# Kernel optimization log

Measured on AMD Instinct MI355X. Metric: run time of the kernel, lower is better.

The kernel has to match this reference:

```python
import jax, jax.numpy as jnp
import numpy as np


def _compute_wavelet(scaling_rec):
    # g_k = h_{M-k-1}, with sign flip on odd indices (note: torch code flips
    # first, then negates odd indices of the flipped filter).
    g = jnp.flip(scaling_rec, axis=-1)
    signs = jnp.where(jnp.arange(g.shape[-1]) % 2 == 1, -1.0, 1.0).astype(g.dtype)
    return g * signs


def _convolve(x, filt):
    # Circular convolution via rFFT, matching torch.fft.rfft/irfft semantics.
    n = x.shape[-1]
    ra = jnp.fft.rfft(x)
    rb = jnp.fft.rfft(filt, n=n)
    return jnp.fft.irfft(ra * rb, n=n).astype(x.dtype)


def setup_inputs() -> dict:
    key = jax.random.key(0)
    k1, k2, k3 = jax.random.split(key, 3)
    inp = jax.random.normal(k1, (4096, 8192), dtype=jnp.float32)
    scaling = jax.random.normal(k2, (8,), dtype=jnp.float32)
    scaling_rec = jax.random.normal(k3, (8,), dtype=jnp.float32)
    return {"input": inp, "scaling": scaling, "scaling_rec": scaling_rec}


def reference(input, scaling, scaling_rec):
    wavelet = _compute_wavelet(scaling_rec)
    even = input[:, ::2]   # (n, m/2)
    odd = input[:, 1::2]   # (n, m/2)
    odd_updated = odd - _convolve(even, wavelet)
    even_updated = even - _convolve(odd, scaling)
    return (even_updated, odd_updated)
```

## Files before the change

kernel.cpp:

```cpp
#include <hip/hip_runtime.h>


#define COLS       8192
#define HALF       4096
#define F4_PER_ROW 2048
#define NTHREADS   256

__global__ __launch_bounds__(NTHREADS) void fwd_dwt_kernel(
    const float* __restrict__ input,
    const float* __restrict__ scaling,
    const float* __restrict__ scaling_rec,
    float* __restrict__ out,
    int rows)
{
    const int t   = blockIdx.x * NTHREADS + threadIdx.x;
    const int row = t >> 11;
    const int f   = t & (F4_PER_ROW - 1);

    const float4* in4 = (const float4*)(input + (size_t)row * COLS);

    float w[8], sc[8];
#pragma unroll
    for (int j = 0; j < 8; ++j) {
        w[j]  = scaling_rec[7 - j] * ((j & 1) ? -1.0f : 1.0f);
        sc[j] = scaling[j];
    }

    const float4 v  = in4[f];
    const float4 h1 = in4[(f - 1) & (F4_PER_ROW - 1)];
    const float4 h2 = in4[(f - 2) & (F4_PER_ROW - 1)];
    const float4 h3 = in4[(f - 3) & (F4_PER_ROW - 1)];
    const float4 h4 = in4[(f - 4) & (F4_PER_ROW - 1)];

    float pe[9], po[9];
    pe[0] = h4.z; po[0] = h4.w;
    pe[1] = h3.x; po[1] = h3.y;  pe[2] = h3.z; po[2] = h3.w;
    pe[3] = h2.x; po[3] = h2.y;  pe[4] = h2.z; po[4] = h2.w;
    pe[5] = h1.x; po[5] = h1.y;  pe[6] = h1.z; po[6] = h1.w;
    pe[7] = v.x;  po[7] = v.y;   pe[8] = v.z;  po[8] = v.w;

    float eo0 = pe[7], oo0 = po[7], eo1 = pe[8], oo1 = po[8];
#pragma unroll
    for (int j = 0; j < 8; ++j) {
        eo0 -= po[7 - j] * sc[j];
        oo0 -= pe[7 - j] * w[j];
        eo1 -= po[8 - j] * sc[j];
        oo1 -= pe[8 - j] * w[j];
    }

    float* oe = out + (size_t)row * HALF + 2 * f;
    float* od = out + (size_t)rows * HALF + (size_t)row * HALF + 2 * f;
    ((float2*)oe)[0] = make_float2(eo0, eo1);
    ((float2*)od)[0] = make_float2(oo0, oo1);
}

extern "C" void kernel_launch(void* const* d_in, const int* in_sizes, int n_in,
                              void* d_out, int out_size, void* d_ws, size_t ws_size,
                              hipStream_t stream) {
    const float* input       = (const float*)d_in[0];
    const float* scaling     = (const float*)d_in[1];
    const float* scaling_rec = (const float*)d_in[2];
    float*       out         = (float*)d_out;

    const int rows    = in_sizes[0] / COLS;
    const int threads = rows * F4_PER_ROW;
    fwd_dwt_kernel<<<threads / NTHREADS, NTHREADS, 0, stream>>>(
        input, scaling, scaling_rec, out, rows);
}
```

Before: 228.7 us.

## Process multiple rows per thread with double-buffered register prefetch

Each thread now handles 16 rows strided by rows/16 instead of one. The next row's five float4 loads are issued before computing the current one, giving a software-pipelined double buffer in registers. The goal is to cut grid size, amortise filter-coefficient loads and index math, and keep more memory requests in flight per thread. In exchange the grid is 16x smaller, which lowers wave-level parallelism and raises register use. The code assumes rows is divisible by 16.

```diff
diff --git a/kernel.cpp b/kernel.cpp
--- a/kernel.cpp
+++ b/kernel.cpp
@@ -5,6 +5,7 @@
 #define HALF       4096
 #define F4_PER_ROW 2048
 #define NTHREADS   256
+#define ITERS      16
 
 __global__ __launch_bounds__(NTHREADS) void fwd_dwt_kernel(
     const float* __restrict__ input,
@@ -13,11 +14,15 @@
     float* __restrict__ out,
     int rows)
 {
-    const int t   = blockIdx.x * NTHREADS + threadIdx.x;
-    const int row = t >> 11;
-    const int f   = t & (F4_PER_ROW - 1);
+    const int g       = blockIdx.x * NTHREADS + threadIdx.x;
+    const int f       = g & (F4_PER_ROW - 1);
+    const int rowbase = g >> 11;
+    const int rs      = rows / ITERS;
 
-    const float4* in4 = (const float4*)(input + (size_t)row * COLS);
+    const int m1 = (f - 1) & (F4_PER_ROW - 1);
+    const int m2 = (f - 2) & (F4_PER_ROW - 1);
+    const int m3 = (f - 3) & (F4_PER_ROW - 1);
+    const int m4 = (f - 4) & (F4_PER_ROW - 1);
 
     float w[8], sc[8];
 #pragma unroll
@@ -26,32 +31,62 @@
         sc[j] = scaling[j];
     }
 
-    const float4 v  = in4[f];
-    const float4 h1 = in4[(f - 1) & (F4_PER_ROW - 1)];
-    const float4 h2 = in4[(f - 2) & (F4_PER_ROW - 1)];
-    const float4 h3 = in4[(f - 3) & (F4_PER_ROW - 1)];
-    const float4 h4 = in4[(f - 4) & (F4_PER_ROW - 1)];
+    struct W5 { float4 v, h1, h2, h3, h4; };
 
-    float pe[9], po[9];
-    pe[0] = h4.z; po[0] = h4.w;
-    pe[1] = h3.x; po[1] = h3.y;  pe[2] = h3.z; po[2] = h3.w;
-    pe[3] = h2.x; po[3] = h2.y;  pe[4] = h2.z; po[4] = h2.w;
-    pe[5] = h1.x; po[5] = h1.y;  pe[6] = h1.z; po[6] = h1.w;
-    pe[7] = v.x;  po[7] = v.y;   pe[8] = v.z;  po[8] = v.w;
+    auto LOAD = [&](const float4* base) {
+        W5 r;
+        r.v  = base[f];
+        r.h1 = base[m1];
+        r.h2 = base[m2];
+        r.h3 = base[m3];
+        r.h4 = base[m4];
+        return r;
+    };
 
-    float eo0 = pe[7], oo0 = po[7], eo1 = pe[8], oo1 = po[8];
+    auto CRUNCH = [&](const W5& x, float* poe, float* pod) {
+        float pe[9], po[9];
+        pe[0] = x.h4.z; po[0] = x.h4.w;
+        pe[1] = x.h3.x; po[1] = x.h3.y;  pe[2] = x.h3.z; po[2] = x.h3.w;
+        pe[3] = x.h2.x; po[3] = x.h2.y;  pe[4] = x.h2.z; po[4] = x.h2.w;
+        pe[5] = x.h1.x; po[5] = x.h1.y;  pe[6] = x.h1.z; po[6] = x.h1.w;
+        pe[7] = x.v.x;  po[7] = x.v.y;   pe[8] = x.v.z;  po[8] = x.v.w;
+
+        float eo0 = pe[7], oo0 = po[7], eo1 = pe[8], oo1 = po[8];
 #pragma unroll
-    for (int j = 0; j < 8; ++j) {
-        eo0 -= po[7 - j] * sc[j];
-        oo0 -= pe[7 - j] * w[j];
-        eo1 -= po[8 - j] * sc[j];
-        oo1 -= pe[8 - j] * w[j];
+        for (int j = 0; j < 8; ++j) {
+            eo0 -= po[7 - j] * sc[j];
+            oo0 -= pe[7 - j] * w[j];
+            eo1 -= po[8 - j] * sc[j];
+            oo1 -= pe[8 - j] * w[j];
+        }
+        ((float2*)poe)[0] = make_float2(eo0, eo1);
+        ((float2*)pod)[0] = make_float2(oo0, oo1);
+    };
+
+    const size_t in_step  = (size_t)rs * F4_PER_ROW;
+    const size_t out_step = (size_t)rs * HALF;
+
+    const float4* ip = (const float4*)input + (size_t)rowbase * F4_PER_ROW;
+    float* pe = out + (size_t)rowbase * HALF + 2 * f;
+    float* po = pe + (size_t)rows * HALF;
+
+    W5 A = LOAD(ip);
+#pragma unroll 1
+    for (int it = 0; it < ITERS; it += 2) {
+        const float4* ip1 = ip + in_step;
+        W5 B = LOAD(ip1);
+
+        CRUNCH(A, pe, po);
+        pe += out_step; po += out_step;
+
+        const float4* ip2 = ip1 + in_step;
+        if (it + 2 < ITERS) A = LOAD(ip2);
+
+        CRUNCH(B, pe, po);
+        pe += out_step; po += out_step;
+
+        ip = ip2;
     }
-
-    float* oe = out + (size_t)row * HALF + 2 * f;
-    float* od = out + (size_t)rows * HALF + (size_t)row * HALF + 2 * f;
-    ((float2*)oe)[0] = make_float2(eo0, eo1);
-    ((float2*)od)[0] = make_float2(oo0, oo1);
 }
 
 extern "C" void kernel_launch(void* const* d_in, const int* in_sizes, int n_in,
@@ -63,7 +98,7 @@
     float*       out         = (float*)d_out;
 
     const int rows    = in_sizes[0] / COLS;
-    const int threads = rows * F4_PER_ROW;
+    const int threads = (rows / ITERS) * F4_PER_ROW;
     fwd_dwt_kernel<<<threads / NTHREADS, NTHREADS, 0, stream>>>(
         input, scaling, scaling_rec, out, rows);
 }
```

New measurement: 235.7 us. 3.0% more time.

## Stage input tiles into LDS via direct global-to-LDS loads with double buffering

Applied to the files above, without the earlier changes.

Each wave now processes 16 rows, loading each row's 64-float4 segment plus a 4-float4 halo straight into LDS with global_load_lds. The next tile's load is issued before the current one is computed, so load latency overlaps compute. Each thread then reads its five neighbouring float4s from LDS instead of issuing five overlapping global loads. This cuts redundant global and L2 traffic and the block count, at the cost of fewer waves in flight, manual vmcnt waits and no barriers (correctness relies on wave-private buffers).

```diff
diff --git a/kernel.cpp b/kernel.cpp
--- a/kernel.cpp
+++ b/kernel.cpp
@@ -1,23 +1,41 @@
 #include <hip/hip_runtime.h>
+#include <stdint.h>
 
 
-#define COLS       8192
-#define HALF       4096
-#define F4_PER_ROW 2048
-#define NTHREADS   256
+#define COLS   8192
+#define HALF   4096
+#define F4R    2048
+#define NT     256
+#define WPB    4
+#define TILES  16
 
-__global__ __launch_bounds__(NTHREADS) void fwd_dwt_kernel(
+typedef const __attribute__((address_space(1))) void* gas_t;
+typedef __attribute__((address_space(3))) void*       las_t;
+
+__global__ __launch_bounds__(NT) void fwd_dwt_kernel(
     const float* __restrict__ input,
     const float* __restrict__ scaling,
     const float* __restrict__ scaling_rec,
     float* __restrict__ out,
     int rows)
 {
-    const int t   = blockIdx.x * NTHREADS + threadIdx.x;
-    const int row = t >> 11;
-    const int f   = t & (F4_PER_ROW - 1);
+    __shared__ float4 lds4[2][WPB][128];
 
-    const float4* in4 = (const float4*)(input + (size_t)row * COLS);
+    const int lane = threadIdx.x & 63;
+    const int widx = threadIdx.x >> 6;
+    const int W    = blockIdx.x * WPB + widx;
+    const int w32  = W & 31;
+    const int row0 = W >> 5;
+    const int F    = w32 * 64 + lane;
+
+    const int ia = (w32 * 64 - 4 + lane) & (F4R - 1);
+    const int ib = (w32 * 64 + 60 + lane) & (F4R - 1);
+
+    const int rs = rows / TILES;
+    const size_t instep = (size_t)rs * F4R;
+
+    const float4* gA = (const float4*)input + (size_t)row0 * F4R + ia;
+    const float4* gB = (const float4*)input + (size_t)row0 * F4R + ib;
 
     float w[8], sc[8];
 #pragma unroll
@@ -26,32 +44,57 @@
         sc[j] = scaling[j];
     }
 
-    const float4 v  = in4[f];
-    const float4 h1 = in4[(f - 1) & (F4_PER_ROW - 1)];
-    const float4 h2 = in4[(f - 2) & (F4_PER_ROW - 1)];
-    const float4 h3 = in4[(f - 3) & (F4_PER_ROW - 1)];
-    const float4 h4 = in4[(f - 4) & (F4_PER_ROW - 1)];
+    auto STAGE = [&](int buf, int t) {
+        const float4* a = gA + (size_t)t * instep;
+        const float4* b = gB + (size_t)t * instep;
+        __builtin_amdgcn_global_load_lds((gas_t)(const void*)a,
+                                         (las_t)(void*)&lds4[buf][widx][0],  16, 0, 0);
+        __builtin_amdgcn_global_load_lds((gas_t)(const void*)b,
+                                         (las_t)(void*)&lds4[buf][widx][64], 16, 0, 0);
+    };
 
-    float pe[9], po[9];
-    pe[0] = h4.z; po[0] = h4.w;
-    pe[1] = h3.x; po[1] = h3.y;  pe[2] = h3.z; po[2] = h3.w;
-    pe[3] = h2.x; po[3] = h2.y;  pe[4] = h2.z; po[4] = h2.w;
-    pe[5] = h1.x; po[5] = h1.y;  pe[6] = h1.z; po[6] = h1.w;
-    pe[7] = v.x;  po[7] = v.y;   pe[8] = v.z;  po[8] = v.w;
+    float* oe = out + (size_t)row0 * HALF + 2 * F;
+    float* od = oe + (size_t)rows * HALF;
+    const size_t ostep = (size_t)rs * HALF;
 
-    float eo0 = pe[7], oo0 = po[7], eo1 = pe[8], oo1 = po[8];
+    STAGE(0, 0);
+
+#pragma unroll 1
+    for (int t = 0; t < TILES; ++t) {
+        const int cur = t & 1;
+        if (t + 1 < TILES) {
+            STAGE(cur ^ 1, t + 1);
+            asm volatile("s_waitcnt vmcnt(2)" ::: "memory");
+        } else {
+            asm volatile("s_waitcnt vmcnt(0)" ::: "memory");
+        }
+
+        const float4 h4 = lds4[cur][widx][lane + 0];
+        const float4 h3 = lds4[cur][widx][lane + 1];
+        const float4 h2 = lds4[cur][widx][lane + 2];
+        const float4 h1 = lds4[cur][widx][lane + 3];
+        const float4 v  = lds4[cur][widx][lane + 4];
+
+        float pe[9], po[9];
+        pe[0] = h4.z; po[0] = h4.w;
+        pe[1] = h3.x; po[1] = h3.y;  pe[2] = h3.z; po[2] = h3.w;
+        pe[3] = h2.x; po[3] = h2.y;  pe[4] = h2.z; po[4] = h2.w;
+        pe[5] = h1.x; po[5] = h1.y;  pe[6] = h1.z; po[6] = h1.w;
+        pe[7] = v.x;  po[7] = v.y;   pe[8] = v.z;  po[8] = v.w;
+
+        float eo0 = pe[7], oo0 = po[7], eo1 = pe[8], oo1 = po[8];
 #pragma unroll
-    for (int j = 0; j < 8; ++j) {
-        eo0 -= po[7 - j] * sc[j];
-        oo0 -= pe[7 - j] * w[j];
-        eo1 -= po[8 - j] * sc[j];
-        oo1 -= pe[8 - j] * w[j];
+        for (int j = 0; j < 8; ++j) {
+            eo0 -= po[7 - j] * sc[j];
+            oo0 -= pe[7 - j] * w[j];
+            eo1 -= po[8 - j] * sc[j];
+            oo1 -= pe[8 - j] * w[j];
+        }
+
+        ((float2*)oe)[0] = make_float2(eo0, eo1);
+        ((float2*)od)[0] = make_float2(oo0, oo1);
+        oe += ostep; od += ostep;
     }
-
-    float* oe = out + (size_t)row * HALF + 2 * f;
-    float* od = out + (size_t)rows * HALF + (size_t)row * HALF + 2 * f;
-    ((float2*)oe)[0] = make_float2(eo0, eo1);
-    ((float2*)od)[0] = make_float2(oo0, oo1);
 }
 
 extern "C" void kernel_launch(void* const* d_in, const int* in_sizes, int n_in,
@@ -62,8 +105,8 @@
     const float* scaling_rec = (const float*)d_in[2];
     float*       out         = (float*)d_out;
 
-    const int rows    = in_sizes[0] / COLS;
-    const int threads = rows * F4_PER_ROW;
-    fwd_dwt_kernel<<<threads / NTHREADS, NTHREADS, 0, stream>>>(
+    const int rows   = in_sizes[0] / COLS;
+    const int blocks = (rows / TILES) * (F4R / 64) / WPB;
+    fwd_dwt_kernel<<<blocks, NT, 0, stream>>>(
         input, scaling, scaling_rec, out, rows);
 }
```

Result: slower. 236.6 us (+3.4%).
